# Kernel tuning notes

Measured on AMD Instinct MI355X. Metric: run time of the kernel, lower is better.

The kernel has to match this reference:

```python
import jax, jax.numpy as jnp
import numpy as np

B, L, HS, NWRD, NTGT, DIM = 8, 128, 1024, 32000, 2000, 128
EPS = 1e-12
T = 1.0  # eval temperature


def setup_inputs() -> dict:
    key = jax.random.key(0)
    ks = jax.random.split(key, 16)
    s = 0.02
    return {
        "inp_word": jax.random.randint(ks[0], (B, L), 0, NWRD, dtype=jnp.int32),
        "masks": jnp.ones((B, L), jnp.float32),
        "spt_mask": jax.random.randint(ks[1], (B, L), 0, 2, dtype=jnp.int32),
        "tgt_ids": jnp.sort(jax.random.randint(ks[2], (NTGT,), 0, NWRD, dtype=jnp.int32)),
        "ctx": jax.random.normal(ks[3], (B, L, HS), jnp.float32),
        "W_spt": jax.random.normal(ks[4], (HS, NTGT), jnp.float32) * s,
        "b_spt": jnp.zeros((NTGT,), jnp.float32),
        "W_nrm": jax.random.normal(ks[5], (HS, NWRD), jnp.float32) * s,
        "b_nrm": jnp.zeros((NWRD,), jnp.float32),
        "W_cpy": jax.random.normal(ks[6], (HS, HS), jnp.float32) * s,
        "b_cpy": jnp.zeros((HS,), jnp.float32),
        "word_emb": jax.random.normal(ks[7], (NWRD, DIM), jnp.float32) * s,
        "word_emb_tgt": jax.random.normal(ks[8], (NTGT, DIM), jnp.float32) * s,
        "g_spt": jax.random.gumbel(ks[9], (B, L, NTGT), jnp.float32),
        "g_nrm": jax.random.gumbel(ks[10], (B, L, NWRD + 1), jnp.float32),
    }


def reference(inp_word, masks, spt_mask, tgt_ids, ctx, W_spt, b_spt, W_nrm, b_nrm,
              W_cpy, b_cpy, word_emb, word_emb_tgt, g_spt, g_nrm):
    spt = spt_mask.astype(jnp.float32)                       # keyword tokens
    nrm = (1.0 - spt) * masks                                # normal (non-pad) tokens

    # special-token head: log(softmax + eps)
    pspt = jnp.log(jax.nn.softmax(jnp.einsum('blh,ht->blt', ctx, W_spt) + b_spt, axis=-1) + EPS)

    # normal head: vocab logits + self copy-attention score
    logits_nrm = jnp.einsum('blh,hv->blv', ctx, W_nrm) + b_nrm           # [B,L,NWRD]
    pcpy = jnp.einsum('blh,blh->bl', jnp.einsum('blh,hk->blk', ctx, W_cpy) + b_cpy, ctx)
    pnrm = jnp.log(jax.nn.softmax(jnp.concatenate([logits_nrm, pcpy[..., None]], axis=-1), axis=-1) + EPS)

    # gumbel-softmax relaxed samples
    sft_spt = jax.nn.softmax((pspt + g_spt) / T, axis=-1)    # [B,L,NTGT]
    sft_nrm = jax.nn.softmax((pnrm + g_nrm) / T, axis=-1)    # [B,L,NWRD+1]

    # hard word choices
    yspt = tgt_ids[jnp.argmax(sft_spt, axis=-1)]
    ynrm_raw = jnp.argmax(sft_nrm, axis=-1).astype(jnp.int32)
    ynrm = jnp.where(ynrm_raw == NWRD, inp_word, ynrm_raw)   # copy fallback
    obf_word = jnp.where(spt > 0, yspt, jnp.where(nrm > 0, ynrm, inp_word))

    # blended embeddings, scatter-combined per token group
    spt_emb = jnp.einsum('blt,td->bld', sft_spt, word_emb_tgt)
    nrm_emb = word_emb[inp_word] * sft_nrm[..., -1:] \
        + jnp.einsum('blv,vd->bld', sft_nrm[..., :-1], word_emb)
    base_emb = word_emb[obf_word]
    obf_word_emb = jnp.where(spt[..., None] > 0, spt_emb,
                             jnp.where(nrm[..., None] > 0, nrm_emb, base_emb))
    return obf_word_emb, obf_word, spt
```

## Files before the change

kernel.cpp:

```cpp
#include <hip/hip_runtime.h>
#include <math.h>

#define TOK   1024
#define HSZ   1024
#define DIM   128
#define NWRDC 32000
#define NTGTC 2000

typedef __attribute__((ext_vector_type(8))) short bf16x8;
typedef __attribute__((ext_vector_type(4))) float f32x4;

__device__ __forceinline__ ushort f2bf(float x) {
    union { float f; uint u; } c; c.f = x;
    return (ushort)((c.u + 0x7fffu + ((c.u >> 16) & 1u)) >> 16);
}
__device__ __forceinline__ float bf2f(ushort h) {
    union { uint u; float f; } c; c.u = ((uint)h) << 16;
    return c.f;
}
__device__ __forceinline__ uint4 pk8(const ushort v[8]) {
    uint4 u;
    u.x = (uint)v[0] | ((uint)v[1] << 16);
    u.y = (uint)v[2] | ((uint)v[3] << 16);
    u.z = (uint)v[4] | ((uint)v[5] << 16);
    u.w = (uint)v[6] | ((uint)v[7] << 16);
    return u;
}

#define GLL16(SRC, DST) __builtin_amdgcn_global_load_lds( \
    (const __attribute__((address_space(1))) void*)(SRC), \
    (__attribute__((address_space(3))) void*)(DST), 16, 0, 0)

__global__ __launch_bounds__(256) void split_ctx3(
    const float* __restrict__ x, ushort* __restrict__ hp,
    ushort* __restrict__ mp, ushort* __restrict__ lp)
{
    const int i4 = (blockIdx.x * 256 + threadIdx.x) * 4;
    float4 v = *(const float4*)(x + i4);
    float xs[4] = {v.x, v.y, v.z, v.w};
    ushort hh[4], mm[4], ll[4];
    #pragma unroll
    for (int k = 0; k < 4; ++k) {
        ushort h = f2bf(xs[k]);
        float r1 = xs[k] - bf2f(h);
        ushort m = f2bf(r1);
        ushort l = f2bf(r1 - bf2f(m));
        hh[k] = h; mm[k] = m; ll[k] = l;
    }
    uint2 u;
    u.x = (uint)hh[0] | ((uint)hh[1] << 16); u.y = (uint)hh[2] | ((uint)hh[3] << 16);
    *(uint2*)(hp + i4) = u;
    u.x = (uint)mm[0] | ((uint)mm[1] << 16); u.y = (uint)mm[2] | ((uint)mm[3] << 16);
    *(uint2*)(mp + i4) = u;
    u.x = (uint)ll[0] | ((uint)ll[1] << 16); u.y = (uint)ll[2] | ((uint)ll[3] << 16);
    *(uint2*)(lp + i4) = u;
}

__device__ __forceinline__ void head_body(
    char* smem, int b, int NVx,
    const ushort* __restrict__ ctx_hi, const ushort* __restrict__ ctx_lo,
    const float* __restrict__ W, const float* __restrict__ bias,
    const float* __restrict__ g, const float* __restrict__ emb,
    int V, int ldg, int tps, int n_tiles,
    float* __restrict__ wsW, float* __restrict__ wsBV,
    int* __restrict__ wsBI, float* __restrict__ wsE)
{
    ushort* Pl = (ushort*)smem;
    ushort* EM = (ushort*)(smem + 34816);
    float* sm_wsum = (float*)(smem + 65536);
    float* sm_bval = (float*)(smem + 66560);
    int*   sm_bidx = (int*)(smem + 67584);

    const int tid  = threadIdx.x;
    const int lane = tid & 63;
    const int fr   = lane & 15;
    const int fg   = lane >> 4;
    const int wv   = tid >> 6;
    const int wrow = wv >> 1;
    const int wcol = wv & 1;
    const int split = b % NVx;
    const int t0    = (b / NVx) * 128;

    if (tid < 128) {
        sm_wsum[tid * 2] = 0.f;        sm_wsum[tid * 2 + 1] = 0.f;
        sm_bval[tid * 2] = -INFINITY;  sm_bval[tid * 2 + 1] = -INFINITY;
        sm_bidx[tid * 2] = 0;          sm_bidx[tid * 2 + 1] = 0;
    }

    const int chunkRd0 = (((fr & 1) << 2) | fg) ^ ((fr >> 1) & 7);
    int aRd[4], bRd[4];
    #pragma unroll
    for (int i = 0; i < 4; ++i) {
        aRd[i] = wrow * 4096 + i * 1024 + (fr >> 1) * 128 + ((chunkRd0 ^ i) << 4);
        bRd[i] = wcol * 4096 + i * 1024 + (fr >> 1) * 128 + ((chunkRd0 ^ i) << 4);
    }

    const int v_    = (lane & 7) ^ (lane >> 3) ^ (wv & 3);
    const int glTok = (wv * 8 + (lane >> 3)) * 2 + (v_ >> 2);
    const int glK   = (v_ & 3) * 8;
    const int glDst = wv * 1024;

    const int c4 = (tid & 31) * 4;
    const int hq = tid >> 5;
    const int kc_w = hq >> 1, half_w = hq & 1;
    int wOff[4];
    #pragma unroll
    for (int i = 0; i < 4; ++i) {
        const int col = c4 + i;
        const int pair = col >> 1;
        const int ch = (((col & 1) << 2) | kc_w) ^ (pair & 7) ^ ((pair >> 3) & 3);
        wOff[i] = pair * 128 + ch * 16 + half_w * 8;
    }

    f32x4 zero4 = {0.f, 0.f, 0.f, 0.f};
    f32x4 Eacc[4][4];
    #pragma unroll
    for (int i = 0; i < 4; ++i)
        #pragma unroll
        for (int j = 0; j < 4; ++j) Eacc[i][j] = zero4;

    int tbeg = split * tps;
    int tend = tbeg + tps; if (tend > n_tiles) tend = n_tiles;

    #define STAGE_A(STEP, BASE) do {                                               \
        const size_t ro_ = (size_t)(t0 + glTok) * HSZ + (size_t)(STEP) * 32 + glK; \
        GLL16(ctx_hi + ro_,          (BASE) + glDst);                              \
        GLL16(ctx_hi + ro_ + 65536,  (BASE) + 4096 + glDst);                       \
        GLL16(ctx_lo + ro_,          (BASE) + 8192 + glDst);                       \
        GLL16(ctx_lo + ro_ + 65536,  (BASE) + 12288 + glDst);                      \
    } while (0)

    #define LOAD_W(STEP, VV) do {                                                 \
        const int gc_ = c0 + c4;                                                   \
        if (gc_ < V) {                                                             \
            const float* p_ = W + (size_t)((STEP) * 32 + hq * 4) * V + gc_;        \
            VV[0] = *(const float4*)p_;                                            \
            VV[1] = *(const float4*)(p_ + V);                                      \
            VV[2] = *(const float4*)(p_ + 2 * (size_t)V);                          \
            VV[3] = *(const float4*)(p_ + 3 * (size_t)V);                          \
        } else {                                                                   \
            float4 z_ = {0.f, 0.f, 0.f, 0.f};                                      \
            VV[0] = z_; VV[1] = z_; VV[2] = z_; VV[3] = z_;                        \
        }                                                                          \
    } while (0)

    #define CONV_W(BH, BL, VV) do {                                               \
        _Pragma("unroll")                                                          \
        for (int i_ = 0; i_ < 4; ++i_) {                                           \
            ushort h_[4], l_[4];                                                   \
            _Pragma("unroll")                                                      \
            for (int q_ = 0; q_ < 4; ++q_) {                                       \
                float x_ = ((const float*)&VV[q_])[i_];                            \
                union { float f; uint u; } c_; c_.f = x_;                          \
                h_[q_] = (ushort)(c_.u >> 16);                                     \
                union { uint u; float f; } t_; t_.u = c_.u & 0xFFFF0000u;          \
                l_[q_] = f2bf(x_ - t_.f);                                          \
            }                                                                      \
            uint2 uh_ = {(uint)h_[0] | ((uint)h_[1] << 16),                        \
                         (uint)h_[2] | ((uint)h_[3] << 16)};                       \
            uint2 ul_ = {(uint)l_[0] | ((uint)l_[1] << 16),                        \
                         (uint)l_[2] | ((uint)l_[3] << 16)};                       \
            *(uint2*)((BH) + wOff[i_]) = uh_;                                      \
            *(uint2*)((BL) + wOff[i_]) = ul_;                                      \
        }                                                                          \
    } while (0)

    for (int tt = tbeg; tt < tend; ++tt) {
        const int c0 = tt * 128;
        f32x4 acc[4][4];
        #pragma unroll
        for (int i = 0; i < 4; ++i)
            #pragma unroll
            for (int j = 0; j < 4; ++j) acc[i][j] = zero4;

        STAGE_A(0, smem);
        {
            float4 v0[4];
            LOAD_W(0, v0);
            CONV_W(smem + 32768, smem + 40960, v0);
        }
        __syncthreads();

        for (int ks = 0; ks < 32; ++ks) {
            const int cur = ks & 1;
            const bool more = (ks + 1) < 32;
            float4 vn[4];
            if (more) {
                STAGE_A(ks + 1, smem + (cur ^ 1) * 16384);
                LOAD_W(ks + 1, vn);
            }
            char* bA = smem + cur * 16384;
            char* bB = smem + 32768 + cur * 16384;
            bf16x8 ah[4], al[4];
            #pragma unroll
            for (int i = 0; i < 4; ++i) {
                ah[i] = *(const bf16x8*)(bA + aRd[i]);
                al[i] = *(const bf16x8*)(bA + 8192 + aRd[i]);
            }
            __builtin_amdgcn_s_setprio(1);
            #pragma unroll
            for (int j = 0; j < 4; ++j) {
                bf16x8 vbh = *(const bf16x8*)(bB + bRd[j]);
                bf16x8 vbl = *(const bf16x8*)(bB + 8192 + bRd[j]);
                #pragma unroll
                for (int i = 0; i < 4; ++i) {
                    acc[i][j] = __builtin_amdgcn_mfma_f32_16x16x32_bf16(ah[i], vbh, acc[i][j], 0, 0, 0);
                    acc[i][j] = __builtin_amdgcn_mfma_f32_16x16x32_bf16(ah[i], vbl, acc[i][j], 0, 0, 0);
                    acc[i][j] = __builtin_amdgcn_mfma_f32_16x16x32_bf16(al[i], vbh, acc[i][j], 0, 0, 0);
                }
            }
            __builtin_amdgcn_s_setprio(0);
            if (more) {
                char* nB = smem + 32768 + (cur ^ 1) * 16384;
                CONV_W(nB, nB + 8192, vn);
            }
            __syncthreads();
        }

        float bias4[4];
        #pragma unroll
        for (int j = 0; j < 4; ++j) {
            const int gc = c0 + wcol * 64 + j * 16 + fr;
            bias4[j] = (gc < V) ? bias[gc] : 0.f;
        }
        #pragma unroll
        for (int i = 0; i < 4; ++i) {
            #pragma unroll
            for (int r = 0; r < 4; ++r) {
                const int trow = wrow * 64 + i * 16 + fg * 4 + r;
                const float* gp = g + (size_t)(t0 + trow) * ldg + c0 + wcol * 64 + fr;
                float esum = 0.f, mx = -INFINITY;
                int mi = 0;
                #pragma unroll
                for (int j = 0; j < 4; ++j) {
                    const int gc = c0 + wcol * 64 + j * 16 + fr;
                    float e = 0.f;
                    if (gc < V) {
                        const float s = acc[i][j][r] + bias4[j] + gp[j * 16];
                        e = __expf(s);
                        esum += e;
                        if (s > mx) { mx = s; mi = gc; }
                    }
                    Pl[trow * 136 + wcol * 64 + j * 16 + fr] = f2bf(e);
                }
                #pragma unroll
                for (int off = 1; off < 16; off <<= 1) {
                    const float ov = __shfl_xor(mx, off, 64);
                    const int   oi = __shfl_xor(mi, off, 64);
                    esum += __shfl_xor(esum, off, 64);
                    if (ov > mx || (ov == mx && oi < mi)) { mx = ov; mi = oi; }
                }
                if (fr == 0) {
                    sm_wsum[trow * 2 + wcol] += esum;
                    const float cb = sm_bval[trow * 2 + wcol];
                    const int   ci = sm_bidx[trow * 2 + wcol];
                    if (mx > cb || (mx == cb && mi < ci)) {
                        sm_bval[trow * 2 + wcol] = mx;
                        sm_bidx[trow * 2 + wcol] = mi;
                    }
                }
            }
        }

        #pragma unroll
        for (int hf = 0; hf < 2; ++hf) {
            __syncthreads();
            #pragma unroll
            for (int rr = 0; rr < 4; ++rr) {
                const int task = tid + rr * 256;
                const int d = task & 127;
                const int cc = task >> 7;
                ushort o8[8];
                #pragma unroll
                for (int j = 0; j < 8; ++j) {
                    const int gc = c0 + hf * 64 + cc * 8 + j;
                    o8[j] = (gc < V) ? f2bf(emb[(size_t)gc * DIM + d]) : (ushort)0;
                }
                *(uint4*)(EM + d * 72 + cc * 8) = pk8(o8);
            }
            __syncthreads();
            #pragma unroll
            for (int ksb = 0; ksb < 2; ++ksb) {
                bf16x8 ap[4];
                #pragma unroll
                for (int i = 0; i < 4; ++i) {
                    const int row = wrow * 64 + i * 16 + fr;
                    ap[i] = *(const bf16x8*)(Pl + row * 136 + hf * 64 + ksb * 32 + fg * 8);
                }
                #pragma unroll
                for (int j = 0; j < 4; ++j) {
                    const int dd = wcol * 64 + j * 16 + fr;
                    bf16x8 eb = *(const bf16x8*)(EM + dd * 72 + ksb * 32 + fg * 8);
                    #pragma unroll
                    for (int i = 0; i < 4; ++i)
                        Eacc[i][j] = __builtin_amdgcn_mfma_f32_16x16x32_bf16(ap[i], eb, Eacc[i][j], 0, 0, 0);
                }
            }
        }
        __syncthreads();
    }

    __syncthreads();
    if (tid < 128) {
        const float wsv = sm_wsum[tid * 2] + sm_wsum[tid * 2 + 1];
        const float b0 = sm_bval[tid * 2], b1 = sm_bval[tid * 2 + 1];
        const int   i0 = sm_bidx[tid * 2], i1 = sm_bidx[tid * 2 + 1];
        float bv; int bi;
        if (b0 > b1 || (b0 == b1 && i0 < i1)) { bv = b0; bi = i0; }
        else                                   { bv = b1; bi = i1; }
        const size_t o = (size_t)split * TOK + t0 + tid;
        wsW[o] = wsv; wsBV[o] = bv; wsBI[o] = bi;
    }
    #pragma unroll
    for (int i = 0; i < 4; ++i)
        #pragma unroll
        for (int j = 0; j < 4; ++j)
            #pragma unroll
            for (int r = 0; r < 4; ++r) {
                const int trow = wrow * 64 + i * 16 + fg * 4 + r;
                const int dd   = wcol * 64 + j * 16 + fr;
                wsE[((size_t)split * TOK + t0 + trow) * DIM + dd] = Eacc[i][j][r];
            }
    #undef STAGE_A
    #undef LOAD_W
    #undef CONV_W
}

__device__ __forceinline__ void cpy_body(
    char* smemc, int cb,
    const ushort* __restrict__ ahi, const ushort* __restrict__ amd,
    const ushort* __restrict__ alo, const float* __restrict__ Wc,
    const float* __restrict__ ctx, const float* __restrict__ bc,
    float* __restrict__ pcpyP)
{
    ushort* sm = (ushort*)smemc;
    ushort* Ah = sm;
    ushort* Am = sm + 5120;
    ushort* Al = sm + 10240;
    ushort* Bh = sm + 15360;
    ushort* Bm = sm + 20480;
    ushort* Bl = sm + 25600;

    const int tid  = threadIdx.x;
    const int lane = tid & 63;
    const int fr   = lane & 15;
    const int fg   = lane >> 4;
    const int w    = tid >> 6;
    const int wrow = w >> 1;
    const int wcol = w & 1;
    const int t0   = (cb >> 3) * 128;
    const int c0   = (cb & 7) * 128;

    const int arow = tid >> 2, akc = tid & 3;
    const int bcol = tid & 127, bkc0 = tid >> 7;

    f32x4 zero4 = {0.f, 0.f, 0.f, 0.f};
    f32x4 acc[4][4];
    #pragma unroll
    for (int i = 0; i < 4; ++i)
        #pragma unroll
        for (int j = 0; j < 4; ++j) acc[i][j] = zero4;

    for (int h0 = 0; h0 < HSZ; h0 += 32) {
        uint4 aH[2], aM[2], aL[2];
        float bx[2][8];
        #pragma unroll
        for (int rr = 0; rr < 2; ++rr) {
            const size_t so = (size_t)(t0 + arow + rr * 64) * HSZ + h0 + akc * 8;
            aH[rr] = *(const uint4*)(ahi + so);
            aM[rr] = *(const uint4*)(amd + so);
            aL[rr] = *(const uint4*)(alo + so);
        }
        #pragma unroll
        for (int rr = 0; rr < 2; ++rr) {
            const int kc = bkc0 + rr * 2;
            const float* wp = Wc + (size_t)(h0 + kc * 8) * HSZ + c0 + bcol;
            #pragma unroll
            for (int j = 0; j < 8; ++j) bx[rr][j] = wp[(size_t)j * HSZ];
        }
        __syncthreads();
        #pragma unroll
        for (int rr = 0; rr < 2; ++rr) {
            const int row = arow + rr * 64;
            *(uint4*)(Ah + row * 40 + akc * 8) = aH[rr];
            *(uint4*)(Am + row * 40 + akc * 8) = aM[rr];
            *(uint4*)(Al + row * 40 + akc * 8) = aL[rr];
        }
        #pragma unroll
        for (int rr = 0; rr < 2; ++rr) {
            const int kc = bkc0 + rr * 2;
            ushort hh[8], mm[8], ll[8];
            #pragma unroll
            for (int j = 0; j < 8; ++j) {
                float x = bx[rr][j];
                ushort h = f2bf(x);
                float r1 = x - bf2f(h);
                ushort m = f2bf(r1);
                hh[j] = h; mm[j] = m; ll[j] = f2bf(r1 - bf2f(m));
            }
            *(uint4*)(Bh + bcol * 40 + kc * 8) = pk8(hh);
            *(uint4*)(Bm + bcol * 40 + kc * 8) = pk8(mm);
            *(uint4*)(Bl + bcol * 40 + kc * 8) = pk8(ll);
        }
        __syncthreads();
        bf16x8 a1[4], a2[4], a3[4];
        #pragma unroll
        for (int i = 0; i < 4; ++i) {
            const int row = wrow * 64 + i * 16 + fr;
            a1[i] = *(const bf16x8*)(Ah + row * 40 + fg * 8);
            a2[i] = *(const bf16x8*)(Am + row * 40 + fg * 8);
            a3[i] = *(const bf16x8*)(Al + row * 40 + fg * 8);
        }
        #pragma unroll
        for (int j = 0; j < 4; ++j) {
            const int cr = wcol * 64 + j * 16 + fr;
            bf16x8 b1 = *(const bf16x8*)(Bh + cr * 40 + fg * 8);
            bf16x8 b2 = *(const bf16x8*)(Bm + cr * 40 + fg * 8);
            bf16x8 b3 = *(const bf16x8*)(Bl + cr * 40 + fg * 8);
            #pragma unroll
            for (int i = 0; i < 4; ++i) {
                acc[i][j] = __builtin_amdgcn_mfma_f32_16x16x32_bf16(a1[i], b1, acc[i][j], 0, 0, 0);
                acc[i][j] = __builtin_amdgcn_mfma_f32_16x16x32_bf16(a1[i], b2, acc[i][j], 0, 0, 0);
                acc[i][j] = __builtin_amdgcn_mfma_f32_16x16x32_bf16(a2[i], b1, acc[i][j], 0, 0, 0);
                acc[i][j] = __builtin_amdgcn_mfma_f32_16x16x32_bf16(a1[i], b3, acc[i][j], 0, 0, 0);
                acc[i][j] = __builtin_amdgcn_mfma_f32_16x16x32_bf16(a3[i], b1, acc[i][j], 0, 0, 0);
                acc[i][j] = __builtin_amdgcn_mfma_f32_16x16x32_bf16(a2[i], b2, acc[i][j], 0, 0, 0);
            }
        }
    }

    __syncthreads();
    float* red = (float*)smemc;
    float bb[4];
    #pragma unroll
    for (int j = 0; j < 4; ++j) bb[j] = bc[c0 + wcol * 64 + j * 16 + fr];
    #pragma unroll
    for (int i = 0; i < 4; ++i) {
        #pragma unroll
        for (int r = 0; r < 4; ++r) {
            const int trow = wrow * 64 + i * 16 + fg * 4 + r;
            const float* cx = ctx + (size_t)(t0 + trow) * HSZ + c0;
            float s = 0.f;
            #pragma unroll
            for (int j = 0; j < 4; ++j) {
                const int dd = wcol * 64 + j * 16 + fr;
                s += (acc[i][j][r] + bb[j]) * cx[dd];
            }
            #pragma unroll
            for (int off = 1; off < 16; off <<= 1) s += __shfl_xor(s, off, 64);
            if (fr == 0) red[trow * 2 + wcol] = s;
        }
    }
    __syncthreads();
    if (tid < 128)
        pcpyP[(size_t)(cb & 7) * TOK + t0 + tid] = red[tid * 2] + red[tid * 2 + 1];
}

__global__ __launch_bounds__(256, 2) void mega_kernel(
    const ushort* __restrict__ ctxh, const ushort* __restrict__ ctxm,
    const ushort* __restrict__ ctxl,
    const float* __restrict__ W_nrm, const float* __restrict__ b_nrm,
    const float* __restrict__ g_nrm, const float* __restrict__ word_emb,
    const float* __restrict__ W_spt, const float* __restrict__ b_spt,
    const float* __restrict__ g_spt, const float* __restrict__ word_emb_tgt,
    const float* __restrict__ W_cpy, const float* __restrict__ b_cpy,
    const float* __restrict__ ctx, float* __restrict__ pcpyP,
    int NVn, int tps_n, int NVs, int tps_s,
    float* __restrict__ nW, float* __restrict__ nBV, int* __restrict__ nBI,
    float* __restrict__ nE,
    float* __restrict__ sW, float* __restrict__ sBV, int* __restrict__ sBI,
    float* __restrict__ sE)
{
    __shared__ __align__(16) char smem[68608];
    const int bid = (int)blockIdx.x;
    const int nbn = NVn * 8, nbs = NVs * 8;
    if (bid < nbn) {
        head_body(smem, bid, NVn, ctxh, ctxm, W_nrm, b_nrm, g_nrm, word_emb,
                  NWRDC, NWRDC + 1, tps_n, NWRDC / 128, nW, nBV, nBI, nE);
    } else if (bid < nbn + nbs) {
        head_body(smem, bid - nbn, NVs, ctxh, ctxm, W_spt, b_spt, g_spt,
                  word_emb_tgt, NTGTC, NTGTC, tps_s, (NTGTC + 127) / 128,
                  sW, sBV, sBI, sE);
    } else {
        cpy_body(smem, bid - nbn - nbs, ctxh, ctxm, ctxl, W_cpy, ctx, b_cpy,
                 pcpyP);
    }
}

__global__ __launch_bounds__(128) void combine_kernel(
    const int* __restrict__ inp_word, const float* __restrict__ masks,
    const int* __restrict__ spt_mask, const int* __restrict__ tgt_ids,
    const float* __restrict__ word_emb, const float* __restrict__ pcpyP,
    const float* __restrict__ g_nrm,
    const float* __restrict__ nW, const float* __restrict__ nBV,
    const int* __restrict__ nBI, const float* __restrict__ nE, int NVn,
    const float* __restrict__ sW, const float* __restrict__ sBV,
    const int* __restrict__ sBI, const float* __restrict__ sE, int NVs,
    float* __restrict__ out)
{
    const int t = (int)blockIdx.x;
    const int d = (int)threadIdx.x;

    float Wn = 0.f, En = 0.f, bv = -INFINITY; int bi = 0;
    for (int v = 0; v < NVn; ++v) {
        const size_t o = (size_t)v * TOK + t;
        Wn += nW[o];
        En += nE[o * DIM + d];
        const float vv = nBV[o]; const int ii = nBI[o];
        if (vv > bv || (vv == bv && ii < bi)) { bv = vv; bi = ii; }
    }
    float pc = 0.f;
    #pragma unroll
    for (int y = 0; y < 8; ++y) pc += pcpyP[(size_t)y * TOK + t];

    const int iw = inp_word[t];
    const float sc = pc + g_nrm[(size_t)t * (NWRDC + 1) + NWRDC];
    const float ec = __expf(sc);
    Wn += ec;
    En += ec * word_emb[(size_t)iw * DIM + d];
    const int ynrm = (sc > bv) ? iw : bi;

    float Ws = 0.f, Ese = 0.f, sv = -INFINITY; int si = 0;
    for (int v = 0; v < NVs; ++v) {
        const size_t o = (size_t)v * TOK + t;
        Ws += sW[o];
        Ese += sE[o * DIM + d];
        const float vv = sBV[o]; const int ii = sBI[o];
        if (vv > sv || (vv == sv && ii < si)) { sv = vv; si = ii; }
    }
    const int yspt = tgt_ids[si];

    const float sptf = (float)spt_mask[t];
    const float nrmf = (1.f - sptf) * masks[t];

    float eo; int obf;
    if (sptf > 0.f)      { eo = Ese / Ws; obf = yspt; }
    else if (nrmf > 0.f) { eo = En / Wn;  obf = ynrm; }
    else                 { obf = iw; eo = word_emb[(size_t)iw * DIM + d]; }

    out[(size_t)t * DIM + d] = eo;
    if (d == 0) {
        out[(size_t)TOK * DIM + t]       = (float)obf;
        out[(size_t)TOK * DIM + TOK + t] = sptf;
    }
}

extern "C" void kernel_launch(void* const* d_in, const int* in_sizes, int n_in,
                              void* d_out, int out_size, void* d_ws, size_t ws_size,
                              hipStream_t stream)
{
    const int*   inp_word = (const int*)d_in[0];
    const float* masks    = (const float*)d_in[1];
    const int*   spt_mask = (const int*)d_in[2];
    const int*   tgt_ids  = (const int*)d_in[3];
    const float* ctx      = (const float*)d_in[4];
    const float* W_spt    = (const float*)d_in[5];
    const float* b_spt    = (const float*)d_in[6];
    const float* W_nrm    = (const float*)d_in[7];
    const float* b_nrm    = (const float*)d_in[8];
    const float* W_cpy    = (const float*)d_in[9];
    const float* b_cpy    = (const float*)d_in[10];
    const float* word_emb = (const float*)d_in[11];
    const float* word_emb_tgt = (const float*)d_in[12];
    const float* g_spt    = (const float*)d_in[13];
    const float* g_nrm    = (const float*)d_in[14];
    float* out = (float*)d_out;

    char* wsb = (char*)d_ws;
    float*  pcpyP = (float*)wsb;
    ushort* ctxh = (ushort*)(wsb + 32768);
    ushort* ctxm = ctxh + 1048576;
    ushort* ctxl = ctxm + 1048576;
    char*   region = wsb + 32768 + 6291456;
    const size_t base = 32768 + 6291456;
    const size_t per_split = (size_t)TOK * (DIM + 3) * 4;

    size_t navail = (ws_size > base + 2 * per_split)
                        ? (ws_size - base) / per_split : 2;
    int NVs = (int)(navail / 5);
    if (NVs < 1) NVs = 1; if (NVs > 8) NVs = 8;
    long rem = (long)navail - NVs;
    int NVn;
    if (rem >= 8) { NVn = (int)(rem & ~7L); if (NVn > 64) NVn = 64; }
    else          { NVn = (rem < 1) ? 1 : (int)rem; }

    float* nW  = (float*)region;
    float* nBV = nW + (size_t)NVn * TOK;
    int*   nBI = (int*)(nBV + (size_t)NVn * TOK);
    float* nE  = (float*)(nBI + (size_t)NVn * TOK);
    float* sW  = nE + (size_t)NVn * TOK * DIM;
    float* sBV = sW + (size_t)NVs * TOK;
    int*   sBI = (int*)(sBV + (size_t)NVs * TOK);
    float* sE  = (float*)(sBI + (size_t)NVs * TOK);

    const int tps_n = (NWRDC / 128 + NVn - 1) / NVn;
    const int ntile_s = (NTGTC + 127) / 128;
    const int tps_s = (ntile_s + NVs - 1) / NVs;

    split_ctx3<<<dim3(TOK * HSZ / 1024), dim3(256), 0, stream>>>(ctx, ctxh, ctxm, ctxl);
    mega_kernel<<<dim3(NVn * 8 + NVs * 8 + 64), dim3(256), 0, stream>>>(
        ctxh, ctxm, ctxl, W_nrm, b_nrm, g_nrm, word_emb,
        W_spt, b_spt, g_spt, word_emb_tgt, W_cpy, b_cpy, ctx, pcpyP,
        NVn, tps_n, NVs, tps_s, nW, nBV, nBI, nE, sW, sBV, sBI, sE);
    combine_kernel<<<dim3(TOK), dim3(128), 0, stream>>>(
        inp_word, masks, spt_mask, tgt_ids, word_emb, pcpyP, g_nrm,
        nW, nBV, nBI, nE, NVn, sW, sBV, sBI, sE, NVs, out);
    (void)in_sizes; (void)n_in; (void)out_size;
}
```

Before: 946.0 us.

## Use single-bf16 GEMM with top-3 candidates and exact fp64 re-score of near ties

The head GEMMs drop the split-bf16 three-MFMA scheme (hi*hi, hi*lo, lo*hi) and use one bf16 product with W rounded to bf16, which cuts MFMA work and LDS traffic to about a third. To keep the argmax correct, each split now tracks the top-3 candidates per token. The combine kernel re-scores candidates in fp64 from the original fp32 ctx and W whenever the top two are within a margin or the copy score is close. Split counts are also reworked into a fixed table. The risk is wrong hard choices when the bf16 error exceeds the margin, and the blended embeddings now use lower-precision probabilities.

```diff
diff --git a/kernel.cpp b/kernel.cpp
--- a/kernel.cpp
+++ b/kernel.cpp
@@ -25,6 +25,15 @@
     u.z = (uint)v[4] | ((uint)v[5] << 16);
     u.w = (uint)v[6] | ((uint)v[7] << 16);
     return u;
+}
+__device__ __forceinline__ void ins3(float v, int ix, float s[3], int ii[3]) {
+    if (v > s[0] || (v == s[0] && ix < ii[0])) {
+        s[2] = s[1]; ii[2] = ii[1]; s[1] = s[0]; ii[1] = ii[0]; s[0] = v; ii[0] = ix;
+    } else if (v > s[1] || (v == s[1] && ix < ii[1])) {
+        s[2] = s[1]; ii[2] = ii[1]; s[1] = v; ii[1] = ix;
+    } else if (v > s[2] || (v == s[2] && ix < ii[2])) {
+        s[2] = v; ii[2] = ix;
+    }
 }
 
 #define GLL16(SRC, DST) __builtin_amdgcn_global_load_lds( \
@@ -58,18 +67,18 @@
 
 __device__ __forceinline__ void head_body(
     char* smem, int b, int NVx,
-    const ushort* __restrict__ ctx_hi, const ushort* __restrict__ ctx_lo,
-    const float* __restrict__ W, const float* __restrict__ bias,
-    const float* __restrict__ g, const float* __restrict__ emb,
-    int V, int ldg, int tps, int n_tiles,
+    const ushort* __restrict__ ctx_hi, const float* __restrict__ W,
+    const float* __restrict__ bias, const float* __restrict__ g,
+    const float* __restrict__ emb,
+    int V, int ldg, int n_tiles,
     float* __restrict__ wsW, float* __restrict__ wsBV,
     int* __restrict__ wsBI, float* __restrict__ wsE)
 {
     ushort* Pl = (ushort*)smem;
     ushort* EM = (ushort*)(smem + 34816);
-    float* sm_wsum = (float*)(smem + 65536);
-    float* sm_bval = (float*)(smem + 66560);
-    int*   sm_bidx = (int*)(smem + 67584);
+    float* sm_wsum = (float*)(smem + 53248);
+    float* sm_bval = (float*)(smem + 54272);
+    int*   sm_bidx = (int*)(smem + 57344);
 
     const int tid  = threadIdx.x;
     const int lane = tid & 63;
@@ -82,9 +91,14 @@
     const int t0    = (b / NVx) * 128;
 
     if (tid < 128) {
-        sm_wsum[tid * 2] = 0.f;        sm_wsum[tid * 2 + 1] = 0.f;
-        sm_bval[tid * 2] = -INFINITY;  sm_bval[tid * 2 + 1] = -INFINITY;
-        sm_bidx[tid * 2] = 0;          sm_bidx[tid * 2 + 1] = 0;
+        sm_wsum[tid * 2] = 0.f; sm_wsum[tid * 2 + 1] = 0.f;
+        #pragma unroll
+        for (int s = 0; s < 3; ++s) {
+            sm_bval[(tid * 2) * 3 + s] = -INFINITY;
+            sm_bval[(tid * 2 + 1) * 3 + s] = -INFINITY;
+            sm_bidx[(tid * 2) * 3 + s] = 0;
+            sm_bidx[(tid * 2 + 1) * 3 + s] = 0;
+        }
     }
 
     const int chunkRd0 = (((fr & 1) << 2) | fg) ^ ((fr >> 1) & 7);
@@ -95,21 +109,27 @@
         bRd[i] = wcol * 4096 + i * 1024 + (fr >> 1) * 128 + ((chunkRd0 ^ i) << 4);
     }
 
-    const int v_    = (lane & 7) ^ (lane >> 3) ^ (wv & 3);
-    const int glTok = (wv * 8 + (lane >> 3)) * 2 + (v_ >> 2);
-    const int glK   = (v_ & 3) * 8;
-    const int glDst = wv * 1024;
+    const int v_ = (lane & 7) ^ (lane >> 3) ^ (wv & 3);
+    int rowq[2];
+    #pragma unroll
+    for (int q = 0; q < 2; ++q)
+        rowq[q] = 2 * (q * 32 + wv * 8 + (lane >> 3)) + (v_ >> 2);
+    const int glK = (v_ & 3) * 8;
+    const size_t srcA0 = (size_t)(t0 + rowq[0]) * HSZ + glK;
+    const size_t srcA1 = (size_t)(t0 + rowq[1]) * HSZ + glK;
+    const int dA0 = wv * 1024, dA1 = 4096 + wv * 1024;
 
     const int c4 = (tid & 31) * 4;
-    const int hq = tid >> 5;
-    const int kc_w = hq >> 1, half_w = hq & 1;
-    int wOff[4];
+    const int hb2 = (tid >> 5) * 2;
+    int wb01[4], wb23[4];
     #pragma unroll
     for (int i = 0; i < 4; ++i) {
         const int col = c4 + i;
         const int pair = col >> 1;
-        const int ch = (((col & 1) << 2) | kc_w) ^ (pair & 7) ^ ((pair >> 3) & 3);
-        wOff[i] = pair * 128 + ch * 16 + half_w * 8;
+        const int ch01 = (((col & 1) << 2) | (hb2 >> 3)) ^ (pair & 7) ^ ((pair >> 3) & 3);
+        const int ch23 = (((col & 1) << 2) | (2 + (hb2 >> 3))) ^ (pair & 7) ^ ((pair >> 3) & 3);
+        wb01[i] = pair * 128 + ch01 * 16 + (hb2 & 7) * 2;
+        wb23[i] = pair * 128 + ch23 * 16 + (hb2 & 7) * 2;
     }
 
     f32x4 zero4 = {0.f, 0.f, 0.f, 0.f};
@@ -119,50 +139,38 @@
         #pragma unroll
         for (int j = 0; j < 4; ++j) Eacc[i][j] = zero4;
 
-    int tbeg = split * tps;
-    int tend = tbeg + tps; if (tend > n_tiles) tend = n_tiles;
-
-    #define STAGE_A(STEP, BASE) do {                                               \
-        const size_t ro_ = (size_t)(t0 + glTok) * HSZ + (size_t)(STEP) * 32 + glK; \
-        GLL16(ctx_hi + ro_,          (BASE) + glDst);                              \
-        GLL16(ctx_hi + ro_ + 65536,  (BASE) + 4096 + glDst);                       \
-        GLL16(ctx_lo + ro_,          (BASE) + 8192 + glDst);                       \
-        GLL16(ctx_lo + ro_ + 65536,  (BASE) + 12288 + glDst);                      \
+    const int tbeg = (split * n_tiles) / NVx;
+    const int tend = ((split + 1) * n_tiles) / NVx;
+
+    #define STAGE_A(STEP, BASE) do {                                    \
+        GLL16(ctx_hi + srcA0 + (size_t)(STEP) * 32, (BASE) + dA0);      \
+        GLL16(ctx_hi + srcA1 + (size_t)(STEP) * 32, (BASE) + dA1);      \
     } while (0)
 
-    #define LOAD_W(STEP, VV) do {                                                 \
-        const int gc_ = c0 + c4;                                                   \
-        if (gc_ < V) {                                                             \
-            const float* p_ = W + (size_t)((STEP) * 32 + hq * 4) * V + gc_;        \
-            VV[0] = *(const float4*)p_;                                            \
-            VV[1] = *(const float4*)(p_ + V);                                      \
-            VV[2] = *(const float4*)(p_ + 2 * (size_t)V);                          \
-            VV[3] = *(const float4*)(p_ + 3 * (size_t)V);                          \
-        } else {                                                                   \
-            float4 z_ = {0.f, 0.f, 0.f, 0.f};                                      \
-            VV[0] = z_; VV[1] = z_; VV[2] = z_; VV[3] = z_;                        \
-        }                                                                          \
+    #define LOAD_W(STEP, VV) do {                                        \
+        const int gc_ = c0 + c4;                                         \
+        if (gc_ + 3 < V) {                                               \
+            const float* p_ = W + (size_t)((STEP) * 32 + hb2) * V + gc_; \
+            VV[0] = *(const float4*)p_;                                  \
+            VV[1] = *(const float4*)(p_ + V);                            \
+            VV[2] = *(const float4*)(p_ + 16 * (size_t)V);               \
+            VV[3] = *(const float4*)(p_ + 17 * (size_t)V);               \
+        } else {                                                         \
+            float4 z_ = {0.f, 0.f, 0.f, 0.f};                            \
+            VV[0] = z_; VV[1] = z_; VV[2] = z_; VV[3] = z_;              \
+        }                                                                \
     } while (0)
 
-    #define CONV_W(BH, BL, VV) do {                                               \
-        _Pragma("unroll")                                                          \
-        for (int i_ = 0; i_ < 4; ++i_) {                                           \
-            ushort h_[4], l_[4];                                                   \
-            _Pragma("unroll")                                                      \
-            for (int q_ = 0; q_ < 4; ++q_) {                                       \
-                float x_ = ((const float*)&VV[q_])[i_];                            \
-                union { float f; uint u; } c_; c_.f = x_;                          \
-                h_[q_] = (ushort)(c_.u >> 16);                                     \
-                union { uint u; float f; } t_; t_.u = c_.u & 0xFFFF0000u;          \
-                l_[q_] = f2bf(x_ - t_.f);                                          \
-            }                                                                      \
-            uint2 uh_ = {(uint)h_[0] | ((uint)h_[1] << 16),                        \
-                         (uint)h_[2] | ((uint)h_[3] << 16)};                       \
-            uint2 ul_ = {(uint)l_[0] | ((uint)l_[1] << 16),                        \
-                         (uint)l_[2] | ((uint)l_[3] << 16)};                       \
-            *(uint2*)((BH) + wOff[i_]) = uh_;                                      \
-            *(uint2*)((BL) + wOff[i_]) = ul_;                                      \
-        }                                                                          \
+    #define CONV_W(BB, VV) do {                                          \
+        _Pragma("unroll")                                                \
+        for (int i_ = 0; i_ < 4; ++i_) {                                 \
+            ushort h0b = f2bf(((const float*)&VV[0])[i_]);               \
+            ushort h1b = f2bf(((const float*)&VV[1])[i_]);               \
+            ushort h2b = f2bf(((const float*)&VV[2])[i_]);               \
+            ushort h3b = f2bf(((const float*)&VV[3])[i_]);               \
+            *(uint*)((BB) + wb01[i_]) = (uint)h0b | ((uint)h1b << 16);   \
+            *(uint*)((BB) + wb23[i_]) = (uint)h2b | ((uint)h3b << 16);   \
+        }                                                                \
     } while (0)
 
     for (int tt = tbeg; tt < tend; ++tt) {
@@ -177,7 +185,7 @@
         {
             float4 v0[4];
             LOAD_W(0, v0);
-            CONV_W(smem + 32768, smem + 40960, v0);
+            CONV_W(smem + 16384, v0);
         }
         __syncthreads();
 
@@ -186,34 +194,24 @@
             const bool more = (ks + 1) < 32;
             float4 vn[4];
             if (more) {
-                STAGE_A(ks + 1, smem + (cur ^ 1) * 16384);
+                STAGE_A(ks + 1, smem + (cur ^ 1) * 8192);
                 LOAD_W(ks + 1, vn);
             }
-            char* bA = smem + cur * 16384;
-            char* bB = smem + 32768 + cur * 16384;
-            bf16x8 ah[4], al[4];
-            #pragma unroll
-            for (int i = 0; i < 4; ++i) {
-                ah[i] = *(const bf16x8*)(bA + aRd[i]);
-                al[i] = *(const bf16x8*)(bA + 8192 + aRd[i]);
-            }
+            const char* bA = smem + cur * 8192;
+            const char* bB = smem + 16384 + cur * 8192;
+            bf16x8 ah[4], bh[4];
+            #pragma unroll
+            for (int i = 0; i < 4; ++i) ah[i] = *(const bf16x8*)(bA + aRd[i]);
+            #pragma unroll
+            for (int j = 0; j < 4; ++j) bh[j] = *(const bf16x8*)(bB + bRd[j]);
             __builtin_amdgcn_s_setprio(1);
             #pragma unroll
-            for (int j = 0; j < 4; ++j) {
-                bf16x8 vbh = *(const bf16x8*)(bB + bRd[j]);
-                bf16x8 vbl = *(const bf16x8*)(bB + 8192 + bRd[j]);
-                #pragma unroll
-                for (int i = 0; i < 4; ++i) {
-                    acc[i][j] = __builtin_amdgcn_mfma_f32_16x16x32_bf16(ah[i], vbh, acc[i][j], 0, 0, 0);
-                    acc[i][j] = __builtin_amdgcn_mfma_f32_16x16x32_bf16(ah[i], vbl, acc[i][j], 0, 0, 0);
-                    acc[i][j] = __builtin_amdgcn_mfma_f32_16x16x32_bf16(al[i], vbh, acc[i][j], 0, 0, 0);
-                }
-            }
+            for (int j = 0; j < 4; ++j)
+                #pragma unroll
+                for (int i = 0; i < 4; ++i)
+                    acc[i][j] = __builtin_amdgcn_mfma_f32_16x16x32_bf16(ah[i], bh[j], acc[i][j], 0, 0, 0);
             __builtin_amdgcn_s_setprio(0);
-            if (more) {
-                char* nB = smem + 32768 + (cur ^ 1) * 16384;
-                CONV_W(nB, nB + 8192, vn);
-            }
+            if (more) CONV_W(smem + 16384 + (cur ^ 1) * 8192, vn);
             __syncthreads();
         }
 
@@ -229,8 +227,9 @@
             for (int r = 0; r < 4; ++r) {
                 const int trow = wrow * 64 + i * 16 + fg * 4 + r;
                 const float* gp = g + (size_t)(t0 + trow) * ldg + c0 + wcol * 64 + fr;
-                float esum = 0.f, mx = -INFINITY;
-                int mi = 0;
+                float esum = 0.f;
+                float t3v[3] = {-INFINITY, -INFINITY, -INFINITY};
+                int   t3i[3] = {0, 0, 0};
                 #pragma unroll
                 for (int j = 0; j < 4; ++j) {
                     const int gc = c0 + wcol * 64 + j * 16 + fr;
@@ -239,25 +238,33 @@
                         const float s = acc[i][j][r] + bias4[j] + gp[j * 16];
                         e = __expf(s);
                         esum += e;
-                        if (s > mx) { mx = s; mi = gc; }
+                        ins3(s, gc, t3v, t3i);
                     }
                     Pl[trow * 136 + wcol * 64 + j * 16 + fr] = f2bf(e);
                 }
                 #pragma unroll
                 for (int off = 1; off < 16; off <<= 1) {
-                    const float ov = __shfl_xor(mx, off, 64);
-                    const int   oi = __shfl_xor(mi, off, 64);
+                    float o0 = __shfl_xor(t3v[0], off, 64);
+                    float o1 = __shfl_xor(t3v[1], off, 64);
+                    float o2 = __shfl_xor(t3v[2], off, 64);
+                    int q0 = __shfl_xor(t3i[0], off, 64);
+                    int q1 = __shfl_xor(t3i[1], off, 64);
+                    int q2 = __shfl_xor(t3i[2], off, 64);
                     esum += __shfl_xor(esum, off, 64);
-                    if (ov > mx || (ov == mx && oi < mi)) { mx = ov; mi = oi; }
+                    ins3(o0, q0, t3v, t3i);
+                    ins3(o1, q1, t3v, t3i);
+                    ins3(o2, q2, t3v, t3i);
                 }
                 if (fr == 0) {
+                    const int sb = (trow * 2 + wcol) * 3;
                     sm_wsum[trow * 2 + wcol] += esum;
-                    const float cb = sm_bval[trow * 2 + wcol];
-                    const int   ci = sm_bidx[trow * 2 + wcol];
-                    if (mx > cb || (mx == cb && mi < ci)) {
-                        sm_bval[trow * 2 + wcol] = mx;
-                        sm_bidx[trow * 2 + wcol] = mi;
-                    }
+                    float sh[3] = {sm_bval[sb], sm_bval[sb + 1], sm_bval[sb + 2]};
+                    int shi[3] = {sm_bidx[sb], sm_bidx[sb + 1], sm_bidx[sb + 2]};
+                    ins3(t3v[0], t3i[0], sh, shi);
+                    ins3(t3v[1], t3i[1], sh, shi);
+                    ins3(t3v[2], t3i[2], sh, shi);
+                    sm_bval[sb] = sh[0]; sm_bval[sb + 1] = sh[1]; sm_bval[sb + 2] = sh[2];
+                    sm_bidx[sb] = shi[0]; sm_bidx[sb + 1] = shi[1]; sm_bidx[sb + 2] = shi[2];
                 }
             }
         }
@@ -268,15 +275,15 @@
             #pragma unroll
             for (int rr = 0; rr < 4; ++rr) {
                 const int task = tid + rr * 256;
-                const int d = task & 127;
+                const int dd0 = task & 127;
                 const int cc = task >> 7;
                 ushort o8[8];
                 #pragma unroll
                 for (int j = 0; j < 8; ++j) {
                     const int gc = c0 + hf * 64 + cc * 8 + j;
-                    o8[j] = (gc < V) ? f2bf(emb[(size_t)gc * DIM + d]) : (ushort)0;
-                }
-                *(uint4*)(EM + d * 72 + cc * 8) = pk8(o8);
+                    o8[j] = (gc < V) ? f2bf(emb[(size_t)gc * DIM + dd0]) : (ushort)0;
+                }
+                *(uint4*)(EM + dd0 * 72 + cc * 8) = pk8(o8);
             }
             __syncthreads();
             #pragma unroll
@@ -302,14 +309,16 @@
 
     __syncthreads();
     if (tid < 128) {
-        const float wsv = sm_wsum[tid * 2] + sm_wsum[tid * 2 + 1];
-        const float b0 = sm_bval[tid * 2], b1 = sm_bval[tid * 2 + 1];
-        const int   i0 = sm_bidx[tid * 2], i1 = sm_bidx[tid * 2 + 1];
-        float bv; int bi;
-        if (b0 > b1 || (b0 == b1 && i0 < i1)) { bv = b0; bi = i0; }
-        else                                   { bv = b1; bi = i1; }
+        const int sb0 = (tid * 2) * 3, sb1 = (tid * 2 + 1) * 3;
+        float v3[3] = {sm_bval[sb0], sm_bval[sb0 + 1], sm_bval[sb0 + 2]};
+        int i3[3] = {sm_bidx[sb0], sm_bidx[sb0 + 1], sm_bidx[sb0 + 2]};
+        ins3(sm_bval[sb1], sm_bidx[sb1], v3, i3);
+        ins3(sm_bval[sb1 + 1], sm_bidx[sb1 + 1], v3, i3);
+        ins3(sm_bval[sb1 + 2], sm_bidx[sb1 + 2], v3, i3);
         const size_t o = (size_t)split * TOK + t0 + tid;
-        wsW[o] = wsv; wsBV[o] = bv; wsBI[o] = bi;
+        wsW[o] = sm_wsum[tid * 2] + sm_wsum[tid * 2 + 1];
+        #pragma unroll
+        for (int s = 0; s < 3; ++s) { wsBV[o * 3 + s] = v3[s]; wsBI[o * 3 + s] = i3[s]; }
     }
     #pragma unroll
     for (int i = 0; i < 4; ++i)
@@ -465,81 +474,152 @@
     const float* __restrict__ g_spt, const float* __restrict__ word_emb_tgt,
     const float* __restrict__ W_cpy, const float* __restrict__ b_cpy,
     const float* __restrict__ ctx, float* __restrict__ pcpyP,
-    int NVn, int tps_n, int NVs, int tps_s,
+    int NVn, int NVs,
     float* __restrict__ nW, float* __restrict__ nBV, int* __restrict__ nBI,
     float* __restrict__ nE,
     float* __restrict__ sW, float* __restrict__ sBV, int* __restrict__ sBI,
     float* __restrict__ sE)
 {
-    __shared__ __align__(16) char smem[68608];
+    __shared__ __align__(16) char smem[61440];
     const int bid = (int)blockIdx.x;
-    const int nbn = NVn * 8, nbs = NVs * 8;
-    if (bid < nbn) {
-        head_body(smem, bid, NVn, ctxh, ctxm, W_nrm, b_nrm, g_nrm, word_emb,
-                  NWRDC, NWRDC + 1, tps_n, NWRDC / 128, nW, nBV, nBI, nE);
-    } else if (bid < nbn + nbs) {
-        head_body(smem, bid - nbn, NVs, ctxh, ctxm, W_spt, b_spt, g_spt,
-                  word_emb_tgt, NTGTC, NTGTC, tps_s, (NTGTC + 127) / 128,
-                  sW, sBV, sBI, sE);
+    if (bid < 64) {
+        cpy_body(smem, bid, ctxh, ctxm, ctxl, W_cpy, ctx, b_cpy, pcpyP);
+    } else if (bid < 64 + NVn * 8) {
+        head_body(smem, bid - 64, NVn, ctxh, W_nrm, b_nrm, g_nrm, word_emb,
+                  NWRDC, NWRDC + 1, 250, nW, nBV, nBI, nE);
     } else {
-        cpy_body(smem, bid - nbn - nbs, ctxh, ctxm, ctxl, W_cpy, ctx, b_cpy,
-                 pcpyP);
-    }
-}
-
-__global__ __launch_bounds__(128) void combine_kernel(
+        head_body(smem, bid - 64 - NVn * 8, NVs, ctxh, W_spt, b_spt, g_spt,
+                  word_emb_tgt, NTGTC, NTGTC, 16, sW, sBV, sBI, sE);
+    }
+}
+
+__global__ __launch_bounds__(128) void combine2(
     const int* __restrict__ inp_word, const float* __restrict__ masks,
     const int* __restrict__ spt_mask, const int* __restrict__ tgt_ids,
     const float* __restrict__ word_emb, const float* __restrict__ pcpyP,
-    const float* __restrict__ g_nrm,
+    const float* __restrict__ g_nrm, const float* __restrict__ g_spt,
+    const float* __restrict__ ctx,
+    const float* __restrict__ b_nrm, const float* __restrict__ b_spt,
+    const float* __restrict__ W_nrm, const float* __restrict__ W_spt,
     const float* __restrict__ nW, const float* __restrict__ nBV,
     const int* __restrict__ nBI, const float* __restrict__ nE, int NVn,
     const float* __restrict__ sW, const float* __restrict__ sBV,
     const int* __restrict__ sBI, const float* __restrict__ sE, int NVs,
     float* __restrict__ out)
 {
+    __shared__ double sredN[2][3];
+    __shared__ double sredS[2][3];
     const int t = (int)blockIdx.x;
     const int d = (int)threadIdx.x;
 
-    float Wn = 0.f, En = 0.f, bv = -INFINITY; int bi = 0;
+    float Wn = 0.f, En = 0.f;
+    float cv[3] = {-INFINITY, -INFINITY, -INFINITY}; int ci[3] = {0, 0, 0};
     for (int v = 0; v < NVn; ++v) {
         const size_t o = (size_t)v * TOK + t;
         Wn += nW[o];
         En += nE[o * DIM + d];
-        const float vv = nBV[o]; const int ii = nBI[o];
-        if (vv > bv || (vv == bv && ii < bi)) { bv = vv; bi = ii; }
-    }
+        #pragma unroll
+        for (int s = 0; s < 3; ++s) ins3(nBV[o * 3 + s], nBI[o * 3 + s], cv, ci);
+    }
+    float Ws = 0.f, Es = 0.f;
+    float dv[3] = {-INFINITY, -INFINITY, -INFINITY}; int di[3] = {0, 0, 0};
+    for (int v = 0; v < NVs; ++v) {
+        const size_t o = (size_t)v * TOK + t;
+        Ws += sW[o];
+        Es += sE[o * DIM + d];
+        #pragma unroll
+        for (int s = 0; s < 3; ++s) ins3(sBV[o * 3 + s], sBI[o * 3 + s], dv, di);
+    }
+
     float pc = 0.f;
     #pragma unroll
     for (int y = 0; y < 8; ++y) pc += pcpyP[(size_t)y * TOK + t];
-
     const int iw = inp_word[t];
     const float sc = pc + g_nrm[(size_t)t * (NWRDC + 1) + NWRDC];
+
+    const float EPS = 0.02f;
+    const bool needN = (cv[0] - cv[1] <= EPS) || (fabsf(sc - cv[0]) <= EPS);
+    const bool needS = (dv[0] - dv[1] <= EPS);
+
+    if (needN || needS) {
+        float cxv[8];
+        #pragma unroll
+        for (int q = 0; q < 8; ++q) cxv[q] = ctx[(size_t)t * HSZ + d * 8 + q];
+        #pragma unroll
+        for (int c = 0; c < 3; ++c) {
+            double p = 0.0;
+            if (needN && cv[c] > -1e30f) {
+                const float* wc = W_nrm + ci[c];
+                #pragma unroll
+                for (int q = 0; q < 8; ++q)
+                    p += (double)cxv[q] * (double)wc[(size_t)(d * 8 + q) * NWRDC];
+            }
+            #pragma unroll
+            for (int off = 32; off > 0; off >>= 1) p += __shfl_down(p, off, 64);
+            if ((d & 63) == 0) sredN[d >> 6][c] = p;
+        }
+        #pragma unroll
+        for (int c = 0; c < 3; ++c) {
+            double p = 0.0;
+            if (needS && dv[c] > -1e30f) {
+                const float* wc = W_spt + di[c];
+                #pragma unroll
+                for (int q = 0; q < 8; ++q)
+                    p += (double)cxv[q] * (double)wc[(size_t)(d * 8 + q) * NTGTC];
+            }
+            #pragma unroll
+            for (int off = 32; off > 0; off >>= 1) p += __shfl_down(p, off, 64);
+            if ((d & 63) == 0) sredS[d >> 6][c] = p;
+        }
+        __syncthreads();
+    }
+
     const float ec = __expf(sc);
     Wn += ec;
     En += ec * word_emb[(size_t)iw * DIM + d];
-    const int ynrm = (sc > bv) ? iw : bi;
-
-    float Ws = 0.f, Ese = 0.f, sv = -INFINITY; int si = 0;
-    for (int v = 0; v < NVs; ++v) {
-        const size_t o = (size_t)v * TOK + t;
-        Ws += sW[o];
-        Ese += sE[o * DIM + d];
-        const float vv = sBV[o]; const int ii = sBI[o];
-        if (vv > sv || (vv == sv && ii < si)) { sv = vv; si = ii; }
-    }
-    const int yspt = tgt_ids[si];
 
     const float sptf = (float)spt_mask[t];
     const float nrmf = (1.f - sptf) * masks[t];
 
-    float eo; int obf;
-    if (sptf > 0.f)      { eo = Ese / Ws; obf = yspt; }
-    else if (nrmf > 0.f) { eo = En / Wn;  obf = ynrm; }
-    else                 { obf = iw; eo = word_emb[(size_t)iw * DIM + d]; }
-
+    float eo;
+    if (sptf > 0.f)      eo = Es / Ws;
+    else if (nrmf > 0.f) eo = En / Wn;
+    else                 eo = word_emb[(size_t)iw * DIM + d];
     out[(size_t)t * DIM + d] = eo;
+
     if (d == 0) {
+        float bnv = cv[0]; int bni = ci[0];
+        if (needN) {
+            bnv = -INFINITY; bni = 0;
+            #pragma unroll
+            for (int c = 0; c < 3; ++c) {
+                if (cv[c] > -1e30f) {
+                    const float s = (float)(sredN[0][c] + sredN[1][c])
+                                  + b_nrm[ci[c]]
+                                  + g_nrm[(size_t)t * (NWRDC + 1) + ci[c]];
+                    if (s > bnv || (s == bnv && ci[c] < bni)) { bnv = s; bni = ci[c]; }
+                }
+            }
+        }
+        float bsv = dv[0]; int bsi = di[0];
+        if (needS) {
+            bsv = -INFINITY; bsi = 0;
+            #pragma unroll
+            for (int c = 0; c < 3; ++c) {
+                if (dv[c] > -1e30f) {
+                    const float s = (float)(sredS[0][c] + sredS[1][c])
+                                  + b_spt[di[c]]
+                                  + g_spt[(size_t)t * NTGTC + di[c]];
+                    if (s > bsv || (s == bsv && di[c] < bsi)) { bsv = s; bsi = di[c]; }
+                }
+            }
+        }
+        const int ynrm = (sc > bnv) ? iw : bni;
+        const int yspt = tgt_ids[bsi];
+        int obf;
+        if (sptf > 0.f)      obf = yspt;
+        else if (nrmf > 0.f) obf = ynrm;
+        else                 obf = iw;
         out[(size_t)TOK * DIM + t]       = (float)obf;
         out[(size_t)TOK * DIM + TOK + t] = sptf;
     }
@@ -573,37 +653,35 @@
     ushort* ctxl = ctxm + 1048576;
     char*   region = wsb + 32768 + 6291456;
     const size_t base = 32768 + 6291456;
-    const size_t per_split = (size_t)TOK * (DIM + 3) * 4;
-
-    size_t navail = (ws_size > base + 2 * per_split)
-                        ? (ws_size - base) / per_split : 2;
-    int NVs = (int)(navail / 5);
-    if (NVs < 1) NVs = 1; if (NVs > 8) NVs = 8;
-    long rem = (long)navail - NVs;
-    int NVn;
-    if (rem >= 8) { NVn = (int)(rem & ~7L); if (NVn > 64) NVn = 64; }
-    else          { NVn = (rem < 1) ? 1 : (int)rem; }
+    const size_t per_split = (size_t)TOK * (1 + 3 + 3 + DIM) * 4;
+
+    int NVn = 1, NVs = 1;
+    {
+        const int tn[8] = {48, 32, 24, 16, 8, 4, 2, 1};
+        const int ts[8] = { 8,  8,  8,  8, 8, 4, 2, 1};
+        for (int pi = 0; pi < 8; ++pi) {
+            const size_t need = base + (size_t)(tn[pi] + ts[pi]) * per_split;
+            if (ws_size >= need) { NVn = tn[pi]; NVs = ts[pi]; break; }
+        }
+    }
 
     float* nW  = (float*)region;
     float* nBV = nW + (size_t)NVn * TOK;
-    int*   nBI = (int*)(nBV + (size_t)NVn * TOK);
-    float* nE  = (float*)(nBI + (size_t)NVn * TOK);
+    int*   nBI = (int*)(nBV + (size_t)NVn * TOK * 3);
+    float* nE  = (float*)(nBI + (size_t)NVn * TOK * 3);
     float* sW  = nE + (size_t)NVn * TOK * DIM;
     float* sBV = sW + (size_t)NVs * TOK;
-    int*   sBI = (int*)(sBV + (size_t)NVs * TOK);
-    float* sE  = (float*)(sBI + (size_t)NVs * TOK);
-
-    const int tps_n = (NWRDC / 128 + NVn - 1) / NVn;
-    const int ntile_s = (NTGTC + 127) / 128;
-    const int tps_s = (ntile_s + NVs - 1) / NVs;
+    int*   sBI = (int*)(sBV + (size_t)NVs * TOK * 3);
+    float* sE  = (float*)(sBI + (size_t)NVs * TOK * 3);
 
     split_ctx3<<<dim3(TOK * HSZ / 1024), dim3(256), 0, stream>>>(ctx, ctxh, ctxm, ctxl);
-    mega_kernel<<<dim3(NVn * 8 + NVs * 8 + 64), dim3(256), 0, stream>>>(
+    mega_kernel<<<dim3(64 + NVn * 8 + NVs * 8), dim3(256), 0, stream>>>(
         ctxh, ctxm, ctxl, W_nrm, b_nrm, g_nrm, word_emb,
         W_spt, b_spt, g_spt, word_emb_tgt, W_cpy, b_cpy, ctx, pcpyP,
-        NVn, tps_n, NVs, tps_s, nW, nBV, nBI, nE, sW, sBV, sBI, sE);
-    combine_kernel<<<dim3(TOK), dim3(128), 0, stream>>>(
-        inp_word, masks, spt_mask, tgt_ids, word_emb, pcpyP, g_nrm,
+        NVn, NVs, nW, nBV, nBI, nE, sW, sBV, sBI, sE);
+    combine2<<<dim3(TOK), dim3(128), 0, stream>>>(
+        inp_word, masks, spt_mask, tgt_ids, word_emb, pcpyP, g_nrm, g_spt, ctx,
+        b_nrm, b_spt, W_nrm, W_spt,
         nW, nBV, nBI, nE, NVn, sW, sBV, sBI, sE, NVs, out);
     (void)in_sizes; (void)n_in; (void)out_size;
 }
```

Result: slower. 1.458 ms (+54.1%).
